# Performance work log

Measured on AMD Instinct MI355X. Metric: run time of the kernel, lower is better.

## Reference

```python
import jax, jax.numpy as jnp
import numpy as np

HIDDEN = 512
HEADS = 8
LN_EPS = 1e-5


def setup_inputs() -> dict:
    key = jax.random.key(0)
    ks = jax.random.split(key, 10)
    n, bsz, h = 128, 4, HIDDEN
    state = jax.random.normal(ks[0], (n, n, bsz, h), dtype=jnp.float32)
    relation = jax.random.normal(ks[1], (n, n, bsz, h), dtype=jnp.float32)
    attn_mask = jnp.zeros((n, bsz, n), dtype=bool)  # key_padding_mask, True = pad
    std = 0.02
    Wq = jax.random.normal(ks[2], (h, h), dtype=jnp.float32) * std
    bq = jnp.zeros((h,), dtype=jnp.float32)
    Wk = jax.random.normal(ks[3], (h, h), dtype=jnp.float32) * std
    bk = jnp.zeros((h,), dtype=jnp.float32)
    Wp = jax.random.normal(ks[4], (h, 2 * h), dtype=jnp.float32) * std
    bp = jnp.zeros((h,), dtype=jnp.float32)
    gamma = jnp.ones((h,), dtype=jnp.float32)
    beta = jnp.zeros((h,), dtype=jnp.float32)
    return {"state": state, "relation": relation, "attn_mask": attn_mask, "n": n,
            "Wq": Wq, "bq": bq, "Wk": Wk, "bk": bk, "Wp": Wp, "bp": bp,
            "gamma": gamma, "beta": beta}


def reference(state, relation, attn_mask, n, Wq, bq, Wk, bk, Wp, bp, gamma, beta):
    # state, relation: [n, n, bsz, h]; attn_mask: [n, bsz, n] (True = pad key)
    h = state.shape[-1]
    dh = h // HEADS
    scale = dh ** -0.5
    # per-row self-attention weights (eval mode: attention dropout is identity)
    q = (jnp.einsum('itbh,oh->itbo', state, Wq) + bq) * scale
    k = jnp.einsum('isbh,oh->isbo', state, Wk) + bk
    qh = q.reshape(q.shape[0], q.shape[1], q.shape[2], HEADS, dh)
    kh = k.reshape(k.shape[0], k.shape[1], k.shape[2], HEADS, dh)
    scores = jnp.einsum('itbnd,isbnd->ibnts', qh, kh)  # [n, bsz, H, t, s]
    pad = attn_mask[:, :, None, None, :]               # [n, bsz, 1, 1, s]
    scores = jnp.where(pad, -jnp.inf, scores)
    probs = jax.nn.softmax(scores, axis=-1)
    w = probs.mean(axis=2)                             # avg over heads -> [n, bsz, t, s]
    # x[i,t,b] = sum_s w[i,b,t,s] * state[i,s,b]
    x = jnp.einsum('ibts,isbh->itbh', w, state)
    # rel_mix[i,t,b] = sum_s w[i,b,t,s] * relation[s,t,b]
    rel_mix = jnp.einsum('ibts,stbh->itbh', w, relation)
    cat = jnp.concatenate([x, rel_mix], axis=-1)       # [n, n, bsz, 2h]
    out = jax.nn.relu(jnp.einsum('itbc,hc->itbh', cat, Wp) + bp)
    # dropout is identity in eval mode; residual + layernorm
    y = state + out
    mu = y.mean(axis=-1, keepdims=True)
    var = y.var(axis=-1, keepdims=True)
    return gamma * (y - mu) * jax.lax.rsqrt(var + LN_EPS) + beta
```

## Files before the change

kernel.cpp:

```cpp
#include <hip/hip_runtime.h>

typedef unsigned short u16;
typedef __attribute__((ext_vector_type(4))) unsigned short u16x4;
typedef __attribute__((ext_vector_type(8))) unsigned short u16x8;
typedef __attribute__((ext_vector_type(8))) short bf16x8;
typedef __attribute__((ext_vector_type(4))) float f32x4;

__device__ __forceinline__ u16 f2bf(float f) {
  union { float f; unsigned u; } v; v.f = f;
  unsigned r = v.u + 0x7fffu + ((v.u >> 16) & 1u);
  return (u16)(r >> 16);
}
__device__ __forceinline__ float bf2f(u16 u) {
  union { unsigned u; float f; } v; v.u = ((unsigned)u) << 16;
  return v.f;
}
__device__ __forceinline__ u16x8 pack8(f32x4 a, f32x4 b) {
  u16x8 r = { f2bf(a.x), f2bf(a.y), f2bf(a.z), f2bf(a.w),
              f2bf(b.x), f2bf(b.y), f2bf(b.z), f2bf(b.w) };
  return r;
}
__device__ __forceinline__ void gload16(const void* g, void* l) {
  __builtin_amdgcn_global_load_lds(
      (const __attribute__((address_space(1))) unsigned int*)g,
      (__attribute__((address_space(3))) unsigned int*)l, 16, 0, 0);
}

__global__ __launch_bounds__(256) void k_prep(
    const float* __restrict__ Wq, const float* __restrict__ Wk,
    const float* __restrict__ bq, const float* __restrict__ bk,
    const float* __restrict__ Wp,
    u16* __restrict__ wqk, u16* __restrict__ wp, float* __restrict__ bqk) {
  int idx = blockIdx.x * 256 + threadIdx.x;
  if (idx < 524288) {
    int o = idx >> 9, hh = idx & 511;
    wqk[idx] = f2bf((o < 512) ? Wq[o * 512 + hh] * 0.125f : Wk[(o - 512) * 512 + hh]);
    wp[idx] = f2bf(Wp[idx]);
  }
  if (idx < 1024) bqk[idx] = (idx < 512) ? bq[idx] * 0.125f : bk[idx - 512];
}

__global__ __launch_bounds__(256) void k_transpose_state(
    const float* __restrict__ src, u16* __restrict__ dst, u16* __restrict__ stB) {
  const int i = blockIdx.z, b = blockIdx.y;
  const int s0 = (blockIdx.x & 1) * 64, h0 = (blockIdx.x >> 1) * 64;
  __shared__ u16 T[64][72];
  const int tid = threadIdx.x;
  const int ls = tid >> 4, lh = (tid & 15) * 4;
#pragma unroll
  for (int rr = 0; rr < 4; ++rr) {
    int s = rr * 16 + ls;
    size_t flat = ((size_t)(i * 128 + s0 + s) * 4 + b) * 512 + h0 + lh;
    f32x4 v = *(const f32x4*)&src[flat];
    u16x4 w4 = { f2bf(v.x), f2bf(v.y), f2bf(v.z), f2bf(v.w) };
    *(u16x4*)&T[s][lh] = w4;
    *(u16x4*)&stB[flat] = w4;
  }
  __syncthreads();
#pragma unroll
  for (int it = 0; it < 2; ++it) {
    int work = it * 256 + tid;
    int hh = work >> 3, sg = (work & 7) * 8;
    u16x8 o;
#pragma unroll
    for (int j = 0; j < 8; ++j) o[j] = T[sg + j][hh];
    *(u16x8*)&dst[((i * 4 + b) * 512 + h0 + hh) * 128 + s0 + sg] = o;
  }
}

__global__ __launch_bounds__(256) void k_qkproj(
    const u16* __restrict__ stB, const u16* __restrict__ wqk,
    const float* __restrict__ bqk, u16* __restrict__ qk) {
  const int flat = blockIdx.x;
  const int xcd = flat & 7, local = flat >> 3;
  const int m0 = (xcd * 64 + (local >> 3)) * 128;
  const int n0 = (local & 7) * 128;
  __shared__ u16 smem[17408];
  u16* As = smem;
  u16* Bs = smem + 8192;
  const int tid = threadIdx.x, lane = tid & 63, wid = tid >> 6;
  const int l15 = lane & 15, l4 = lane >> 4;
  const int wm = (wid >> 1) * 64, wn = (wid & 1) * 64;
  const int lr = lane >> 3;
  const int lcs = ((lane & 7) ^ lr) * 8;
  const int s7 = l15 & 7;
  const f32x4 fz = {0.f, 0.f, 0.f, 0.f};
  f32x4 acc[4][4];
#pragma unroll
  for (int a = 0; a < 4; ++a)
#pragma unroll
    for (int c = 0; c < 4; ++c) acc[a][c] = fz;
  for (int k0 = 0; k0 < 512; k0 += 64) {
    if (k0) __syncthreads();
#pragma unroll
    for (int j = 0; j < 4; ++j) {
      int rb = wid * 32 + j * 8;
      gload16(&stB[(size_t)(m0 + rb + lr) * 512 + k0 + lcs], &As[rb * 64]);
      gload16(&wqk[(size_t)(n0 + rb + lr) * 512 + k0 + lcs], &Bs[rb * 64]);
    }
    __syncthreads();
#pragma unroll
    for (int kk = 0; kk < 64; kk += 32) {
      const int cshift = (((kk >> 3) + l4) ^ s7) * 8;
      bf16x8 af[4], bfr[4];
#pragma unroll
      for (int mf = 0; mf < 4; ++mf)
        af[mf] = *(const bf16x8*)&As[(wm + mf * 16 + l15) * 64 + cshift];
#pragma unroll
      for (int nf = 0; nf < 4; ++nf)
        bfr[nf] = *(const bf16x8*)&Bs[(wn + nf * 16 + l15) * 64 + cshift];
#pragma unroll
      for (int mf = 0; mf < 4; ++mf)
#pragma unroll
        for (int nf = 0; nf < 4; ++nf)
          acc[mf][nf] = __builtin_amdgcn_mfma_f32_16x16x32_bf16(af[mf], bfr[nf], acc[mf][nf], 0, 0, 0);
    }
  }
  float bias[4];
#pragma unroll
  for (int nf = 0; nf < 4; ++nf) bias[nf] = bqk[n0 + wn + nf * 16 + l15];
  __syncthreads();
  u16* Cs = smem;
#pragma unroll
  for (int mf = 0; mf < 4; ++mf)
#pragma unroll
    for (int nf = 0; nf < 4; ++nf)
#pragma unroll
      for (int r = 0; r < 4; ++r)
        Cs[(wm + mf * 16 + l4 * 4 + r) * 136 + wn + nf * 16 + l15] =
            f2bf(acc[mf][nf][r] + bias[nf]);
  __syncthreads();
#pragma unroll
  for (int rr = 0; rr < 8; ++rr) {
    int row = rr * 16 + (tid >> 4), c8 = (tid & 15) * 8;
    *(u16x8*)&qk[(size_t)(m0 + row) * 1024 + n0 + c8] = *(const u16x8*)&Cs[row * 136 + c8];
  }
}

__global__ __launch_bounds__(256) void k_scores(
    const u16* __restrict__ qk, const unsigned char* __restrict__ mask,
    u16* __restrict__ wbuf) {
  const int i = blockIdx.x, b = blockIdx.y;
  __shared__ u16 smem[2 * 128 * 72];
  u16* qs = smem;
  u16* ks = smem + 128 * 72;
  const int tid = threadIdx.x, lane = tid & 63, wid = tid >> 6;
  const int l15 = lane & 15, l4 = lane >> 4;
  float wacc[2][8][4];
#pragma unroll
  for (int mf = 0; mf < 2; ++mf)
#pragma unroll
    for (int nf = 0; nf < 8; ++nf)
#pragma unroll
      for (int r = 0; r < 4; ++r) wacc[mf][nf][r] = 0.f;
  bool mk[8];
#pragma unroll
  for (int nf = 0; nf < 8; ++nf) mk[nf] = mask[i * 512 + b * 128 + nf * 16 + l15] != 0;
  const int arow = tid >> 3, acol = (tid & 7) * 8;
  const f32x4 fz = {0.f, 0.f, 0.f, 0.f};
  for (int h = 0; h < 8; ++h) {
    __syncthreads();
#pragma unroll
    for (int rr = 0; rr < 4; ++rr) {
      int row = rr * 32 + arow;
      int base = ((i * 128 + row) * 4 + b) * 1024 + h * 64 + acol;
      *(u16x8*)&qs[row * 72 + acol] = *(const u16x8*)&qk[base];
      *(u16x8*)&ks[row * 72 + acol] = *(const u16x8*)&qk[base + 512];
    }
    __syncthreads();
#pragma unroll
    for (int mf = 0; mf < 2; ++mf) {
      f32x4 sc[8];
#pragma unroll
      for (int nf = 0; nf < 8; ++nf) sc[nf] = fz;
#pragma unroll
      for (int kk = 0; kk < 64; kk += 32) {
        bf16x8 a = *(const bf16x8*)&qs[(wid * 32 + mf * 16 + l15) * 72 + kk + l4 * 8];
#pragma unroll
        for (int nf = 0; nf < 8; ++nf) {
          bf16x8 bb = *(const bf16x8*)&ks[(nf * 16 + l15) * 72 + kk + l4 * 8];
          sc[nf] = __builtin_amdgcn_mfma_f32_16x16x32_bf16(a, bb, sc[nf], 0, 0, 0);
        }
      }
#pragma unroll
      for (int r = 0; r < 4; ++r) {
        float mx = -3e38f;
#pragma unroll
        for (int nf = 0; nf < 8; ++nf) mx = fmaxf(mx, mk[nf] ? -3e38f : sc[nf][r]);
#pragma unroll
        for (int d = 1; d < 16; d <<= 1) mx = fmaxf(mx, __shfl_xor(mx, d, 64));
        float p[8], sum = 0.f;
#pragma unroll
        for (int nf = 0; nf < 8; ++nf) {
          p[nf] = mk[nf] ? 0.f : __expf(sc[nf][r] - mx);
          sum += p[nf];
        }
#pragma unroll
        for (int d = 1; d < 16; d <<= 1) sum += __shfl_xor(sum, d, 64);
        float inv = 0.125f / sum;
#pragma unroll
        for (int nf = 0; nf < 8; ++nf) wacc[mf][nf][r] += p[nf] * inv;
      }
    }
  }
#pragma unroll
  for (int mf = 0; mf < 2; ++mf)
#pragma unroll
    for (int nf = 0; nf < 8; ++nf)
#pragma unroll
      for (int r = 0; r < 4; ++r) {
        int t = wid * 32 + mf * 16 + l4 * 4 + r;
        wbuf[((i * 4 + b) * 128 + t) * 128 + nf * 16 + l15] = f2bf(wacc[mf][nf][r]);
      }
}

__global__ __launch_bounds__(256) void k_xmix(
    const u16* __restrict__ stT, const u16* __restrict__ wbuf,
    u16* __restrict__ xbuf) {
  const int i = blockIdx.x, b = blockIdx.y, hc = blockIdx.z;
  __shared__ u16 smem[2 * 128 * 136];
  u16* ST = smem;
  u16* WS = smem + 128 * 136;
  const int tid = threadIdx.x, lane = tid & 63, wid = tid >> 6;
  const int l15 = lane & 15, l4 = lane >> 4;
  const int wh = (wid >> 1) * 64, wt = (wid & 1) * 64;
  const f32x4 fz = {0.f, 0.f, 0.f, 0.f};
  f32x4 acc[4][4];
#pragma unroll
  for (int a = 0; a < 4; ++a)
#pragma unroll
    for (int c = 0; c < 4; ++c) acc[a][c] = fz;
  const int r16 = tid >> 4, c8 = (tid & 15) * 8;
#pragma unroll
  for (int rr = 0; rr < 8; ++rr) {
    int row = rr * 16 + r16;
    *(u16x8*)&ST[row * 136 + c8] =
        *(const u16x8*)&stT[((i * 4 + b) * 512 + hc * 128 + row) * 128 + c8];
    *(u16x8*)&WS[row * 136 + c8] =
        *(const u16x8*)&wbuf[((i * 4 + b) * 128 + row) * 128 + c8];
  }
  __syncthreads();
#pragma unroll
  for (int kk = 0; kk < 128; kk += 32) {
    bf16x8 af[4], bfr[4];
#pragma unroll
    for (int mf = 0; mf < 4; ++mf)
      af[mf] = *(const bf16x8*)&ST[(wh + mf * 16 + l15) * 136 + kk + l4 * 8];
#pragma unroll
    for (int nf = 0; nf < 4; ++nf)
      bfr[nf] = *(const bf16x8*)&WS[(wt + nf * 16 + l15) * 136 + kk + l4 * 8];
#pragma unroll
    for (int mf = 0; mf < 4; ++mf)
#pragma unroll
      for (int nf = 0; nf < 4; ++nf)
        acc[mf][nf] = __builtin_amdgcn_mfma_f32_16x16x32_bf16(af[mf], bfr[nf], acc[mf][nf], 0, 0, 0);
  }
  __syncthreads();
  u16* Cs = smem;
#pragma unroll
  for (int mf = 0; mf < 4; ++mf)
#pragma unroll
    for (int nf = 0; nf < 4; ++nf) {
      int h0 = wh + mf * 16 + l4 * 4;
      int t = wt + nf * 16 + l15;
      u16x4 pk = { f2bf(acc[mf][nf][0]), f2bf(acc[mf][nf][1]),
                   f2bf(acc[mf][nf][2]), f2bf(acc[mf][nf][3]) };
      *(u16x4*)&Cs[t * 136 + h0] = pk;
    }
  __syncthreads();
#pragma unroll
  for (int rr = 0; rr < 8; ++rr) {
    int t = rr * 16 + r16;
    *(u16x8*)&xbuf[((i * 128 + t) * 4 + b) * 512 + hc * 128 + c8] =
        *(const u16x8*)&Cs[t * 136 + c8];
  }
}

__global__ __launch_bounds__(256) void k_relmix(
    const float* __restrict__ relation, const u16* __restrict__ wbuf,
    u16* __restrict__ relbuf) {
  const int t = blockIdx.x, b = blockIdx.y, hc = blockIdx.z;
  __shared__ u16 smem[2 * 128 * 136];
  u16* RT = smem;
  u16* WS = smem + 128 * 136;
  u16* T = WS;
  const int tid = threadIdx.x, lane = tid & 63, wid = tid >> 6;
  const int l15 = lane & 15, l4 = lane >> 4;
  const int wh = (wid >> 1) * 64, wi = (wid & 1) * 64;
  const int sr = tid >> 3, hseg = (tid & 7) * 16;
  const int th = tid >> 1, sseg = (tid & 1) * 16;
#pragma unroll
  for (int ch = 0; ch < 4; ++ch) {
    const int sbase = ch * 32;
    size_t gaddr = (((size_t)(sbase + sr) * 128 + t) * 4 + b) * 512 + hc * 128 + hseg;
    f32x4 v0 = *(const f32x4*)&relation[gaddr];
    f32x4 v1 = *(const f32x4*)&relation[gaddr + 4];
    f32x4 v2 = *(const f32x4*)&relation[gaddr + 8];
    f32x4 v3 = *(const f32x4*)&relation[gaddr + 12];
    __syncthreads();
    *(u16x8*)&T[sr * 136 + hseg] = pack8(v0, v1);
    *(u16x8*)&T[sr * 136 + hseg + 8] = pack8(v2, v3);
    __syncthreads();
    u16x8 c0, c1;
#pragma unroll
    for (int j = 0; j < 8; ++j) c0[j] = T[(sseg + j) * 136 + th];
#pragma unroll
    for (int j = 0; j < 8; ++j) c1[j] = T[(sseg + 8 + j) * 136 + th];
    *(u16x8*)&RT[th * 136 + sbase + sseg] = c0;
    *(u16x8*)&RT[th * 136 + sbase + sseg + 8] = c1;
  }
  __syncthreads();
  const int r16 = tid >> 4, c8 = (tid & 15) * 8;
#pragma unroll
  for (int rr = 0; rr < 8; ++rr) {
    int row = rr * 16 + r16;
    *(u16x8*)&WS[row * 136 + c8] =
        *(const u16x8*)&wbuf[((row * 4 + b) * 128 + t) * 128 + c8];
  }
  __syncthreads();
  const f32x4 fz = {0.f, 0.f, 0.f, 0.f};
  f32x4 acc[4][4];
#pragma unroll
  for (int a = 0; a < 4; ++a)
#pragma unroll
    for (int c = 0; c < 4; ++c) acc[a][c] = fz;
#pragma unroll
  for (int kk = 0; kk < 128; kk += 32) {
    bf16x8 af[4], bfr[4];
#pragma unroll
    for (int mf = 0; mf < 4; ++mf)
      af[mf] = *(const bf16x8*)&RT[(wh + mf * 16 + l15) * 136 + kk + l4 * 8];
#pragma unroll
    for (int nf = 0; nf < 4; ++nf)
      bfr[nf] = *(const bf16x8*)&WS[(wi + nf * 16 + l15) * 136 + kk + l4 * 8];
#pragma unroll
    for (int mf = 0; mf < 4; ++mf)
#pragma unroll
      for (int nf = 0; nf < 4; ++nf)
        acc[mf][nf] = __builtin_amdgcn_mfma_f32_16x16x32_bf16(af[mf], bfr[nf], acc[mf][nf], 0, 0, 0);
  }
  __syncthreads();
  u16* Cs = smem;
#pragma unroll
  for (int mf = 0; mf < 4; ++mf)
#pragma unroll
    for (int nf = 0; nf < 4; ++nf) {
      int h0 = wh + mf * 16 + l4 * 4;
      int ii = wi + nf * 16 + l15;
      u16x4 pk = { f2bf(acc[mf][nf][0]), f2bf(acc[mf][nf][1]),
                   f2bf(acc[mf][nf][2]), f2bf(acc[mf][nf][3]) };
      *(u16x4*)&Cs[ii * 136 + h0] = pk;
    }
  __syncthreads();
#pragma unroll
  for (int rr = 0; rr < 8; ++rr) {
    int ii = rr * 16 + r16;
    *(u16x8*)&relbuf[((ii * 128 + t) * 4 + b) * 512 + hc * 128 + c8] =
        *(const u16x8*)&Cs[ii * 136 + c8];
  }
}

__global__ __launch_bounds__(256) void k_proj(
    const u16* __restrict__ xbuf, const u16* __restrict__ relbuf,
    const u16* __restrict__ wp, const float* __restrict__ bp,
    u16* __restrict__ yb) {
  const int flat = blockIdx.x;
  const int xcd = flat & 7, local = flat >> 3;
  const int m0 = (xcd * 64 + (local >> 2)) * 128;
  const int n0 = (local & 3) * 128;
  __shared__ u16 smem[17408];
  u16* As = smem;
  u16* Bs = smem + 8192;
  const int tid = threadIdx.x, lane = tid & 63, wid = tid >> 6;
  const int l15 = lane & 15, l4 = lane >> 4;
  const int wm = (wid >> 1) * 64, wn = (wid & 1) * 64;
  const int lr = lane >> 3;
  const int lcs = ((lane & 7) ^ lr) * 8;
  const int s7 = l15 & 7;
  const f32x4 fz = {0.f, 0.f, 0.f, 0.f};
  f32x4 acc[4][4];
#pragma unroll
  for (int a = 0; a < 4; ++a)
#pragma unroll
    for (int c = 0; c < 4; ++c) acc[a][c] = fz;
  for (int k0 = 0; k0 < 1024; k0 += 64) {
    if (k0) __syncthreads();
    const u16* abase = (k0 < 512) ? xbuf + k0 : relbuf + (k0 - 512);
#pragma unroll
    for (int j = 0; j < 4; ++j) {
      int rb = wid * 32 + j * 8;
      gload16(&abase[(size_t)(m0 + rb + lr) * 512 + lcs], &As[rb * 64]);
      gload16(&wp[(size_t)(n0 + rb + lr) * 1024 + k0 + lcs], &Bs[rb * 64]);
    }
    __syncthreads();
#pragma unroll
    for (int kk = 0; kk < 64; kk += 32) {
      const int cshift = (((kk >> 3) + l4) ^ s7) * 8;
      bf16x8 af[4], bfr[4];
#pragma unroll
      for (int mf = 0; mf < 4; ++mf)
        af[mf] = *(const bf16x8*)&As[(wm + mf * 16 + l15) * 64 + cshift];
#pragma unroll
      for (int nf = 0; nf < 4; ++nf)
        bfr[nf] = *(const bf16x8*)&Bs[(wn + nf * 16 + l15) * 64 + cshift];
#pragma unroll
      for (int mf = 0; mf < 4; ++mf)
#pragma unroll
        for (int nf = 0; nf < 4; ++nf)
          acc[mf][nf] = __builtin_amdgcn_mfma_f32_16x16x32_bf16(af[mf], bfr[nf], acc[mf][nf], 0, 0, 0);
    }
  }
  float bias[4];
#pragma unroll
  for (int nf = 0; nf < 4; ++nf) bias[nf] = bp[n0 + wn + nf * 16 + l15];
  __syncthreads();
  u16* Cs = smem;
#pragma unroll
  for (int mf = 0; mf < 4; ++mf)
#pragma unroll
    for (int nf = 0; nf < 4; ++nf)
#pragma unroll
      for (int r = 0; r < 4; ++r)
        Cs[(wm + mf * 16 + l4 * 4 + r) * 136 + wn + nf * 16 + l15] =
            f2bf(fmaxf(acc[mf][nf][r] + bias[nf], 0.f));
  __syncthreads();
#pragma unroll
  for (int rr = 0; rr < 8; ++rr) {
    int row = rr * 16 + (tid >> 4), c8 = (tid & 15) * 8;
    *(u16x8*)&yb[(size_t)(m0 + row) * 512 + n0 + c8] = *(const u16x8*)&Cs[row * 136 + c8];
  }
}

__global__ __launch_bounds__(256) void k_ln(
    const u16* __restrict__ yb, const float* __restrict__ state,
    const float* __restrict__ gamma, const float* __restrict__ beta,
    float* __restrict__ out) {
  const int tid = threadIdx.x, lane = tid & 63, wid = tid >> 6;
  f32x4 g0 = *(const f32x4*)&gamma[lane * 8];
  f32x4 g1 = *(const f32x4*)&gamma[lane * 8 + 4];
  f32x4 be0 = *(const f32x4*)&beta[lane * 8];
  f32x4 be1 = *(const f32x4*)&beta[lane * 8 + 4];
  for (int row = blockIdx.x * 4 + wid; row < 65536; row += gridDim.x * 4) {
    size_t gbase = (size_t)row * 512 + lane * 8;
    u16x8 yv = *(const u16x8*)&yb[gbase];
    f32x4 s0 = *(const f32x4*)&state[gbase];
    f32x4 s1 = *(const f32x4*)&state[gbase + 4];
    float y[8];
#pragma unroll
    for (int j = 0; j < 4; ++j) y[j] = bf2f(yv[j]) + s0[j];
#pragma unroll
    for (int j = 0; j < 4; ++j) y[4 + j] = bf2f(yv[4 + j]) + s1[j];
    float sum = 0.f, sq = 0.f;
#pragma unroll
    for (int j = 0; j < 8; ++j) { sum += y[j]; sq += y[j] * y[j]; }
#pragma unroll
    for (int d = 1; d < 64; d <<= 1) { sum += __shfl_xor(sum, d, 64); sq += __shfl_xor(sq, d, 64); }
    float mu = sum * (1.f / 512.f);
    float var = sq * (1.f / 512.f) - mu * mu;
    float rs = rsqrtf(var + 1e-5f);
    f32x4 o0, o1;
#pragma unroll
    for (int j = 0; j < 4; ++j) o0[j] = g0[j] * (y[j] - mu) * rs + be0[j];
#pragma unroll
    for (int j = 0; j < 4; ++j) o1[j] = g1[j] * (y[4 + j] - mu) * rs + be1[j];
    *(f32x4*)&out[gbase] = o0;
    *(f32x4*)&out[gbase + 4] = o1;
  }
}

extern "C" void kernel_launch(void* const* d_in, const int* in_sizes, int n_in,
                              void* d_out, int out_size, void* d_ws, size_t ws_size,
                              hipStream_t stream) {
  const float* state = (const float*)d_in[0];
  const float* relation = (const float*)d_in[1];
  const unsigned char* mask = (const unsigned char*)d_in[2];
  const float* Wq = (const float*)d_in[4];
  const float* bq = (const float*)d_in[5];
  const float* Wk = (const float*)d_in[6];
  const float* bk = (const float*)d_in[7];
  const float* Wp = (const float*)d_in[8];
  const float* bp = (const float*)d_in[9];
  const float* gamma = (const float*)d_in[10];
  const float* beta = (const float*)d_in[11];
  float* out = (float*)d_out;
  char* ws = (char*)d_ws;

  u16* qk     = (u16*)(ws);
  u16* xbuf   = (u16*)(ws);
  u16* relbuf = (u16*)(ws + 67108864);
  u16* stT    = (u16*)(ws + 134217728);
  u16* yb     = (u16*)(ws + 134217728);
  u16* stB    = (u16*)(ws + 201326592);
  u16* wbuf   = (u16*)(ws + 268435456);
  u16* wqk    = (u16*)(ws + 285212672);
  u16* wp     = (u16*)(ws + 286261248);
  float* bqk  = (float*)(ws + 287309824);

  k_prep<<<2048, 256, 0, stream>>>(Wq, Wk, bq, bk, Wp, wqk, wp, bqk);
  k_transpose_state<<<dim3(16, 4, 128), 256, 0, stream>>>(state, stT, stB);
  k_qkproj<<<4096, 256, 0, stream>>>(stB, wqk, bqk, qk);
  k_scores<<<dim3(128, 4), 256, 0, stream>>>(qk, mask, wbuf);
  k_xmix<<<dim3(128, 4, 4), 256, 0, stream>>>(stT, wbuf, xbuf);
  k_relmix<<<dim3(128, 4, 4), 256, 0, stream>>>(relation, wbuf, relbuf);
  k_proj<<<2048, 256, 0, stream>>>(xbuf, relbuf, wp, bp, yb);
  k_ln<<<2048, 256, 0, stream>>>(yb, state, gamma, beta, out);
}
```

Baseline: 416.6 us.

## Drop global state transpose, transpose in LDS inside xmix, bf16 residual in LN

Replaces the transpose kernel with a plain fp32-to-bf16 cast, so the transposed stT copy is no longer written to or read from global memory. k_xmix now transposes its state tile in LDS from stB. k_scores moves to 512 threads with one 16-row tile per wave, which doubles the waves per block. k_ln reads the bf16 copy of state instead of fp32 for the residual, halving that read but rounding the residual and adding a small accuracy risk.

```diff
diff --git a/kernel.cpp b/kernel.cpp
--- a/kernel.cpp
+++ b/kernel.cpp
@@ -40,32 +40,12 @@
   if (idx < 1024) bqk[idx] = (idx < 512) ? bq[idx] * 0.125f : bk[idx - 512];
 }
 
-__global__ __launch_bounds__(256) void k_transpose_state(
-    const float* __restrict__ src, u16* __restrict__ dst, u16* __restrict__ stB) {
-  const int i = blockIdx.z, b = blockIdx.y;
-  const int s0 = (blockIdx.x & 1) * 64, h0 = (blockIdx.x >> 1) * 64;
-  __shared__ u16 T[64][72];
-  const int tid = threadIdx.x;
-  const int ls = tid >> 4, lh = (tid & 15) * 4;
-#pragma unroll
-  for (int rr = 0; rr < 4; ++rr) {
-    int s = rr * 16 + ls;
-    size_t flat = ((size_t)(i * 128 + s0 + s) * 4 + b) * 512 + h0 + lh;
-    f32x4 v = *(const f32x4*)&src[flat];
-    u16x4 w4 = { f2bf(v.x), f2bf(v.y), f2bf(v.z), f2bf(v.w) };
-    *(u16x4*)&T[s][lh] = w4;
-    *(u16x4*)&stB[flat] = w4;
-  }
-  __syncthreads();
-#pragma unroll
-  for (int it = 0; it < 2; ++it) {
-    int work = it * 256 + tid;
-    int hh = work >> 3, sg = (work & 7) * 8;
-    u16x8 o;
-#pragma unroll
-    for (int j = 0; j < 8; ++j) o[j] = T[sg + j][hh];
-    *(u16x8*)&dst[((i * 4 + b) * 512 + h0 + hh) * 128 + s0 + sg] = o;
-  }
+__global__ __launch_bounds__(256) void k_cast(
+    const float* __restrict__ src, u16* __restrict__ dst) {
+  size_t idx = ((size_t)blockIdx.x * 256 + threadIdx.x) * 8;
+  f32x4 v0 = *(const f32x4*)&src[idx];
+  f32x4 v1 = *(const f32x4*)&src[idx + 4];
+  *(u16x8*)&dst[idx] = pack8(v0, v1);
 }
 
 __global__ __launch_bounds__(256) void k_qkproj(
@@ -137,7 +117,7 @@
   }
 }
 
-__global__ __launch_bounds__(256) void k_scores(
+__global__ __launch_bounds__(512) void k_scores(
     const u16* __restrict__ qk, const unsigned char* __restrict__ mask,
     u16* __restrict__ wbuf) {
   const int i = blockIdx.x, b = blockIdx.y;
@@ -146,13 +126,11 @@
   u16* ks = smem + 128 * 72;
   const int tid = threadIdx.x, lane = tid & 63, wid = tid >> 6;
   const int l15 = lane & 15, l4 = lane >> 4;
-  float wacc[2][8][4];
-#pragma unroll
-  for (int mf = 0; mf < 2; ++mf)
-#pragma unroll
-    for (int nf = 0; nf < 8; ++nf)
-#pragma unroll
-      for (int r = 0; r < 4; ++r) wacc[mf][nf][r] = 0.f;
+  float wacc[8][4];
+#pragma unroll
+  for (int nf = 0; nf < 8; ++nf)
+#pragma unroll
+    for (int r = 0; r < 4; ++r) wacc[nf][r] = 0.f;
   bool mk[8];
 #pragma unroll
   for (int nf = 0; nf < 8; ++nf) mk[nf] = mask[i * 512 + b * 128 + nf * 16 + l15] != 0;
@@ -161,85 +139,100 @@
   for (int h = 0; h < 8; ++h) {
     __syncthreads();
 #pragma unroll
-    for (int rr = 0; rr < 4; ++rr) {
-      int row = rr * 32 + arow;
+    for (int rr = 0; rr < 2; ++rr) {
+      int row = rr * 64 + arow;
       int base = ((i * 128 + row) * 4 + b) * 1024 + h * 64 + acol;
       *(u16x8*)&qs[row * 72 + acol] = *(const u16x8*)&qk[base];
       *(u16x8*)&ks[row * 72 + acol] = *(const u16x8*)&qk[base + 512];
     }
     __syncthreads();
-#pragma unroll
-    for (int mf = 0; mf < 2; ++mf) {
-      f32x4 sc[8];
-#pragma unroll
-      for (int nf = 0; nf < 8; ++nf) sc[nf] = fz;
-#pragma unroll
-      for (int kk = 0; kk < 64; kk += 32) {
-        bf16x8 a = *(const bf16x8*)&qs[(wid * 32 + mf * 16 + l15) * 72 + kk + l4 * 8];
-#pragma unroll
-        for (int nf = 0; nf < 8; ++nf) {
-          bf16x8 bb = *(const bf16x8*)&ks[(nf * 16 + l15) * 72 + kk + l4 * 8];
-          sc[nf] = __builtin_amdgcn_mfma_f32_16x16x32_bf16(a, bb, sc[nf], 0, 0, 0);
-        }
+    f32x4 sc[8];
+#pragma unroll
+    for (int nf = 0; nf < 8; ++nf) sc[nf] = fz;
+#pragma unroll
+    for (int kk = 0; kk < 64; kk += 32) {
+      bf16x8 a = *(const bf16x8*)&qs[(wid * 16 + l15) * 72 + kk + l4 * 8];
+#pragma unroll
+      for (int nf = 0; nf < 8; ++nf) {
+        bf16x8 bb = *(const bf16x8*)&ks[(nf * 16 + l15) * 72 + kk + l4 * 8];
+        sc[nf] = __builtin_amdgcn_mfma_f32_16x16x32_bf16(a, bb, sc[nf], 0, 0, 0);
       }
-#pragma unroll
-      for (int r = 0; r < 4; ++r) {
-        float mx = -3e38f;
-#pragma unroll
-        for (int nf = 0; nf < 8; ++nf) mx = fmaxf(mx, mk[nf] ? -3e38f : sc[nf][r]);
-#pragma unroll
-        for (int d = 1; d < 16; d <<= 1) mx = fmaxf(mx, __shfl_xor(mx, d, 64));
-        float p[8], sum = 0.f;
-#pragma unroll
-        for (int nf = 0; nf < 8; ++nf) {
-          p[nf] = mk[nf] ? 0.f : __expf(sc[nf][r] - mx);
-          sum += p[nf];
-        }
-#pragma unroll
-        for (int d = 1; d < 16; d <<= 1) sum += __shfl_xor(sum, d, 64);
-        float inv = 0.125f / sum;
-#pragma unroll
-        for (int nf = 0; nf < 8; ++nf) wacc[mf][nf][r] += p[nf] * inv;
+    }
+#pragma unroll
+    for (int r = 0; r < 4; ++r) {
+      float mx = -3e38f;
+#pragma unroll
+      for (int nf = 0; nf < 8; ++nf) mx = fmaxf(mx, mk[nf] ? -3e38f : sc[nf][r]);
+#pragma unroll
+      for (int d = 1; d < 16; d <<= 1) mx = fmaxf(mx, __shfl_xor(mx, d, 64));
+      float p[8], sum = 0.f;
+#pragma unroll
+      for (int nf = 0; nf < 8; ++nf) {
+        p[nf] = mk[nf] ? 0.f : __expf(sc[nf][r] - mx);
+        sum += p[nf];
       }
-    }
-  }
-#pragma unroll
-  for (int mf = 0; mf < 2; ++mf)
-#pragma unroll
-    for (int nf = 0; nf < 8; ++nf)
-#pragma unroll
-      for (int r = 0; r < 4; ++r) {
-        int t = wid * 32 + mf * 16 + l4 * 4 + r;
-        wbuf[((i * 4 + b) * 128 + t) * 128 + nf * 16 + l15] = f2bf(wacc[mf][nf][r]);
-      }
+#pragma unroll
+      for (int d = 1; d < 16; d <<= 1) sum += __shfl_xor(sum, d, 64);
+      float inv = 0.125f / sum;
+#pragma unroll
+      for (int nf = 0; nf < 8; ++nf) wacc[nf][r] += p[nf] * inv;
+    }
+  }
+#pragma unroll
+  for (int nf = 0; nf < 8; ++nf)
+#pragma unroll
+    for (int r = 0; r < 4; ++r) {
+      int t = wid * 16 + l4 * 4 + r;
+      wbuf[((i * 4 + b) * 128 + t) * 128 + nf * 16 + l15] = f2bf(wacc[nf][r]);
+    }
 }
 
 __global__ __launch_bounds__(256) void k_xmix(
-    const u16* __restrict__ stT, const u16* __restrict__ wbuf,
+    const u16* __restrict__ stB, const u16* __restrict__ wbuf,
     u16* __restrict__ xbuf) {
   const int i = blockIdx.x, b = blockIdx.y, hc = blockIdx.z;
   __shared__ u16 smem[2 * 128 * 136];
   u16* ST = smem;
   u16* WS = smem + 128 * 136;
+  u16* T = WS;
   const int tid = threadIdx.x, lane = tid & 63, wid = tid >> 6;
   const int l15 = lane & 15, l4 = lane >> 4;
   const int wh = (wid >> 1) * 64, wt = (wid & 1) * 64;
+  const int sr = tid >> 3, hseg = (tid & 7) * 16;
+  const int th = tid >> 1, sseg = (tid & 1) * 16;
+#pragma unroll
+  for (int ch = 0; ch < 4; ++ch) {
+    const int sbase = ch * 32;
+    size_t gaddr = ((size_t)(i * 128 + sbase + sr) * 4 + b) * 512 + hc * 128 + hseg;
+    u16x8 r0 = *(const u16x8*)&stB[gaddr];
+    u16x8 r1 = *(const u16x8*)&stB[gaddr + 8];
+    __syncthreads();
+    *(u16x8*)&T[sr * 136 + hseg] = r0;
+    *(u16x8*)&T[sr * 136 + hseg + 8] = r1;
+    __syncthreads();
+    u16x8 c0, c1;
+#pragma unroll
+    for (int j = 0; j < 8; ++j) c0[j] = T[(sseg + j) * 136 + th];
+#pragma unroll
+    for (int j = 0; j < 8; ++j) c1[j] = T[(sseg + 8 + j) * 136 + th];
+    *(u16x8*)&ST[th * 136 + sbase + sseg] = c0;
+    *(u16x8*)&ST[th * 136 + sbase + sseg + 8] = c1;
+  }
+  __syncthreads();
+  const int r16 = tid >> 4, c8 = (tid & 15) * 8;
+#pragma unroll
+  for (int rr = 0; rr < 8; ++rr) {
+    int row = rr * 16 + r16;
+    *(u16x8*)&WS[row * 136 + c8] =
+        *(const u16x8*)&wbuf[((i * 4 + b) * 128 + row) * 128 + c8];
+  }
+  __syncthreads();
   const f32x4 fz = {0.f, 0.f, 0.f, 0.f};
   f32x4 acc[4][4];
 #pragma unroll
   for (int a = 0; a < 4; ++a)
 #pragma unroll
     for (int c = 0; c < 4; ++c) acc[a][c] = fz;
-  const int r16 = tid >> 4, c8 = (tid & 15) * 8;
-#pragma unroll
-  for (int rr = 0; rr < 8; ++rr) {
-    int row = rr * 16 + r16;
-    *(u16x8*)&ST[row * 136 + c8] =
-        *(const u16x8*)&stT[((i * 4 + b) * 512 + hc * 128 + row) * 128 + c8];
-    *(u16x8*)&WS[row * 136 + c8] =
-        *(const u16x8*)&wbuf[((i * 4 + b) * 128 + row) * 128 + c8];
-  }
-  __syncthreads();
 #pragma unroll
   for (int kk = 0; kk < 128; kk += 32) {
     bf16x8 af[4], bfr[4];
@@ -432,7 +425,7 @@
 }
 
 __global__ __launch_bounds__(256) void k_ln(
-    const u16* __restrict__ yb, const float* __restrict__ state,
+    const u16* __restrict__ yb, const u16* __restrict__ stB,
     const float* __restrict__ gamma, const float* __restrict__ beta,
     float* __restrict__ out) {
   const int tid = threadIdx.x, lane = tid & 63, wid = tid >> 6;
@@ -443,13 +436,10 @@
   for (int row = blockIdx.x * 4 + wid; row < 65536; row += gridDim.x * 4) {
     size_t gbase = (size_t)row * 512 + lane * 8;
     u16x8 yv = *(const u16x8*)&yb[gbase];
-    f32x4 s0 = *(const f32x4*)&state[gbase];
-    f32x4 s1 = *(const f32x4*)&state[gbase + 4];
+    u16x8 sv = *(const u16x8*)&stB[gbase];
     float y[8];
 #pragma unroll
-    for (int j = 0; j < 4; ++j) y[j] = bf2f(yv[j]) + s0[j];
-#pragma unroll
-    for (int j = 0; j < 4; ++j) y[4 + j] = bf2f(yv[4 + j]) + s1[j];
+    for (int j = 0; j < 8; ++j) y[j] = bf2f(yv[j]) + bf2f(sv[j]);
     float sum = 0.f, sq = 0.f;
 #pragma unroll
     for (int j = 0; j < 8; ++j) { sum += y[j]; sq += y[j] * y[j]; }
@@ -488,7 +478,6 @@
   u16* qk     = (u16*)(ws);
   u16* xbuf   = (u16*)(ws);
   u16* relbuf = (u16*)(ws + 67108864);
-  u16* stT    = (u16*)(ws + 134217728);
   u16* yb     = (u16*)(ws + 134217728);
   u16* stB    = (u16*)(ws + 201326592);
   u16* wbuf   = (u16*)(ws + 268435456);
@@ -497,11 +486,11 @@
   float* bqk  = (float*)(ws + 287309824);
 
   k_prep<<<2048, 256, 0, stream>>>(Wq, Wk, bq, bk, Wp, wqk, wp, bqk);
-  k_transpose_state<<<dim3(16, 4, 128), 256, 0, stream>>>(state, stT, stB);
+  k_cast<<<16384, 256, 0, stream>>>(state, stB);
   k_qkproj<<<4096, 256, 0, stream>>>(stB, wqk, bqk, qk);
-  k_scores<<<dim3(128, 4), 256, 0, stream>>>(qk, mask, wbuf);
-  k_xmix<<<dim3(128, 4, 4), 256, 0, stream>>>(stT, wbuf, xbuf);
+  k_scores<<<dim3(128, 4), 512, 0, stream>>>(qk, mask, wbuf);
+  k_xmix<<<dim3(128, 4, 4), 256, 0, stream>>>(stB, wbuf, xbuf);
   k_relmix<<<dim3(128, 4, 4), 256, 0, stream>>>(relation, wbuf, relbuf);
   k_proj<<<2048, 256, 0, stream>>>(xbuf, relbuf, wp, bp, yb);
-  k_ln<<<2048, 256, 0, stream>>>(yb, state, gamma, beta, out);
-}
+  k_ln<<<2048, 256, 0, stream>>>(yb, stB, gamma, beta, out);
+}
```

Result: faster. 377.4 us (-9.4%).
